# Optimization experiments

Measured on AMD Instinct MI355X. Metric: run time of the kernel, lower is better.

Reference implementation:

```python
import jax, jax.numpy as jnp
import numpy as np

N = 100000      # nodes
E = 1200000     # edges
F_IN = 256      # features_num
HID = 64        # hidden_dim = max(64, 2*32)
NC = 32         # num_class
H = 2           # GAT heads (edge_num < 1.4M)
GAT_SLOPE = 0.2 # GATConv internal LeakyReLU
ACT_SLOPE = 0.01  # F.leaky_relu default


def _glorot(k, shape):
    lim = float(np.sqrt(6.0 / (shape[0] + shape[-1])))
    return jax.random.uniform(k, shape, minval=-lim, maxval=lim, dtype=jnp.float32)


def setup_inputs() -> dict:
    key = jax.random.key(0)
    ks = jax.random.split(key, 32)
    inp = {
        "x": jax.random.normal(ks[0], (N, F_IN), dtype=jnp.float32),
        "edge_index": jax.random.randint(ks[1], (2, E), 0, N, dtype=jnp.int32),
        "edge_weight": jax.random.uniform(ks[2], (E,), dtype=jnp.float32),
    }
    in_dims = [F_IN, 3 * HID]  # layer2 input is cell.output_dim = HID*(1+H)
    ki = 3
    for l, d in enumerate(in_dims):
        inp[f"pre_W{l}"] = _glorot(ks[ki], (d, HID)); ki += 1
        inp[f"pre_b{l}"] = jnp.zeros((HID,), jnp.float32)
        inp[f"gat_W{l}"] = _glorot(ks[ki], (HID, H * HID)); ki += 1
        inp[f"att_src{l}"] = _glorot(ks[ki], (H, HID)); ki += 1
        inp[f"att_dst{l}"] = _glorot(ks[ki], (H, HID)); ki += 1
        inp[f"gat_b{l}"] = jnp.zeros((H * HID,), jnp.float32)
        inp[f"sg_W{l}"] = _glorot(ks[ki], (HID, HID)); ki += 1
        inp[f"sg_b{l}"] = jnp.zeros((HID,), jnp.float32)
    inp["cls_W"] = _glorot(ks[ki], (3 * HID, NC))
    inp["cls_b"] = jnp.zeros((NC,), jnp.float32)
    return inp


def _gat_conv(x, src, dst, W, att_src, att_dst, b):
    # src/dst already include self-loops. x: [N, HID]
    xp = (x @ W).reshape(N, H, HID)                       # [N, H, C]
    a_src = jnp.sum(xp * att_src, axis=-1)                # [N, H]
    a_dst = jnp.sum(xp * att_dst, axis=-1)                # [N, H]
    e = jax.nn.leaky_relu(a_src[src] + a_dst[dst], GAT_SLOPE)  # [E', H]
    m = jax.ops.segment_max(e, dst, num_segments=N)       # segment softmax over dst
    e = jnp.exp(e - m[dst])
    s = jax.ops.segment_sum(e, dst, num_segments=N)
    alpha = e / (s[dst] + 1e-16)
    out = jax.ops.segment_sum(xp[src] * alpha[:, :, None], dst, num_segments=N)
    return out.reshape(N, H * HID) + b


def _sg_conv(x, src_sl, dst_sl, w_sl, W, b):
    # gcn_norm with self-loops (weight 1) already appended; K=1 propagation then linear
    deg = jax.ops.segment_sum(w_sl, dst_sl, num_segments=N)
    dinv = jnp.where(deg > 0, jax.lax.rsqrt(deg), 0.0)
    norm = dinv[src_sl] * w_sl * dinv[dst_sl]             # [E']
    h = jax.ops.segment_sum(x[src_sl] * norm[:, None], dst_sl, num_segments=N)
    return h @ W + b


def _forward(x, edge_index, edge_weight, params):
    src, dst = edge_index[0], edge_index[1]
    loop = jnp.arange(N, dtype=src.dtype)
    src_sl = jnp.concatenate([src, loop])
    dst_sl = jnp.concatenate([dst, loop])
    w_sl = jnp.concatenate([edge_weight, jnp.ones((N,), edge_weight.dtype)])
    for l in range(2):
        pre_W, pre_b, gat_W, a_s, a_d, gat_b, sg_W, sg_b = params[l]
        xh = x @ pre_W + pre_b                            # preprocessor_x
        o1 = jax.nn.leaky_relu(_gat_conv(xh, src_sl, dst_sl, gat_W, a_s, a_d, gat_b), ACT_SLOPE)
        o2 = jax.nn.leaky_relu(_sg_conv(xh, src_sl, dst_sl, w_sl, sg_W, sg_b), ACT_SLOPE)
        x = jax.nn.relu(jnp.concatenate([o1, o2], axis=1))  # [N, 3*HID]
    cls_W, cls_b = params[2]
    logits = x @ cls_W + cls_b
    return jax.nn.log_softmax(logits, axis=-1)


def reference(x, edge_index, edge_weight,
              pre_W0, pre_b0, gat_W0, att_src0, att_dst0, gat_b0, sg_W0, sg_b0,
              pre_W1, pre_b1, gat_W1, att_src1, att_dst1, gat_b1, sg_W1, sg_b1,
              cls_W, cls_b):
    params = [
        (pre_W0, pre_b0, gat_W0, att_src0, att_dst0, gat_b0, sg_W0, sg_b0),
        (pre_W1, pre_b1, gat_W1, att_src1, att_dst1, gat_b1, sg_W1, sg_b1),
        (cls_W, cls_b),
    ]
    return _forward(x, edge_index, edge_weight, params)
```

## Files before the change

### kernel.cpp

```cpp
#include <hip/hip_runtime.h>
#include <hip/hip_fp16.h>
#include <math.h>

#define NN 100000
#define NE 1200000
#define FIN 256
#define NBLK 391
#define HB 4688
#define WB 170
#define GB64 1563

using half8   = __attribute__((ext_vector_type(8))) _Float16;
using floatx4 = __attribute__((ext_vector_type(4))) float;

__device__ __forceinline__ floatx4 mfma16(half8 a, half8 b, floatx4 c) {
    return __builtin_amdgcn_mfma_f32_16x16x32_f16(a, b, c, 0, 0, 0);
}

__device__ __forceinline__ void pre_epi(floatx4* acc, const float* b, const float* attf,
                                        float* asd, float* a_dst, __half* out,
                                        int rowb, int q, int n) {
    float vs0[4] = {0,0,0,0}, vs1[4] = {0,0,0,0};
    float vd0[4] = {0,0,0,0}, vd1[4] = {0,0,0,0};
    #pragma unroll
    for (int t = 0; t < 4; ++t) {
        float bb  = b[t * 16 + n];
        float ws0 = attf[t * 16 + n],       ws1 = attf[64 + t * 16 + n];
        float wd0 = attf[128 + t * 16 + n], wd1 = attf[192 + t * 16 + n];
        #pragma unroll
        for (int r = 0; r < 4; ++r) {
            float xv = acc[t][r] + bb;
            int row = rowb + q * 4 + r;
            if (row < NN) out[(size_t)row * 64 + t * 16 + n] = __float2half(xv);
            vs0[r] = fmaf(xv, ws0, vs0[r]);
            vs1[r] = fmaf(xv, ws1, vs1[r]);
            vd0[r] = fmaf(xv, wd0, vd0[r]);
            vd1[r] = fmaf(xv, wd1, vd1[r]);
        }
    }
    #pragma unroll
    for (int off = 1; off < 16; off <<= 1) {
        #pragma unroll
        for (int r = 0; r < 4; ++r) {
            vs0[r] += __shfl_xor(vs0[r], off);
            vs1[r] += __shfl_xor(vs1[r], off);
            vd0[r] += __shfl_xor(vd0[r], off);
            vd1[r] += __shfl_xor(vd1[r], off);
        }
    }
    if (n == 0) {
        #pragma unroll
        for (int r = 0; r < 4; ++r) {
            int row = rowb + q * 4 + r;
            if (row < NN) {
                *(float2*)&asd[row * 4] = make_float2(vs0[r], vs1[r]);
                *(float2*)&a_dst[row * 2] = make_float2(vd0[r], vd1[r]);
            }
        }
    }
}

__global__ __launch_bounds__(256) void k_prep(const int* __restrict__ dst,
                                              const float* __restrict__ ew,
                                              unsigned long long* __restrict__ packed,
                                              int* __restrict__ ord,
                                              const float* __restrict__ x,
                                              const float* __restrict__ W0,
                                              const float* __restrict__ W1,
                                              const float* __restrict__ Wg0,
                                              const float* __restrict__ Ws0,
                                              const float* __restrict__ Wg1,
                                              const float* __restrict__ Ws1,
                                              const float* __restrict__ Wc,
                                              const float* __restrict__ As0,
                                              const float* __restrict__ Ad0,
                                              const float* __restrict__ As1,
                                              const float* __restrict__ Ad1,
                                              const float* __restrict__ pre_b0,
                                              __half* __restrict__ Wf,
                                              float* __restrict__ attf,
                                              float* __restrict__ asd,
                                              float* __restrict__ a_dst,
                                              __half* __restrict__ xh) {
    __shared__ __half Wl[16384];
    __shared__ float attL[256];
    int bid = blockIdx.x;
    int tid = threadIdx.x;
    if (bid < HB) {
        int e = bid * 256 + tid;
        if (e >= NE) return;
        int d = dst[e]; float w = ew[e];
        unsigned long long add = (1ULL << 48)
            + (unsigned long long)((double)w * 4294967296.0);
        unsigned long long old = atomicAdd(&packed[d], add);
        ord[e] = (int)(old >> 48);
        return;
    }
    if (bid < HB + WB) {
        int o = (bid - HB) * 256 + tid + 16384;
        if (o >= 59904) return;
        if (o >= 59392) {
            int idx = o - 59392;
            int layer = idx >> 8, rem = idx & 255;
            int v = rem >> 6, c = rem & 63, h = v & 1;
            const float* Wg = layer ? Wg1 : Wg0;
            const float* av = (v < 2) ? (layer ? As1 : As0) : (layer ? Ad1 : Ad0);
            float s = 0.f;
            for (int jj = 0; jj < 64; ++jj)
                s = fmaf(Wg[c * 128 + h * 64 + jj], av[h * 64 + jj], s);
            attf[idx] = s;
            return;
        }
        int lo, NT, N; const float* Wg; const float* Wsg = nullptr;
        if (o < 28672)      { lo = o - 16384; NT = 4;  N = 64; Wg = W1; }
        else if (o < 40960) { lo = o - 28672; NT = 12; N = 0;  Wg = Wg0; Wsg = Ws0; }
        else if (o < 53248) { lo = o - 40960; NT = 12; N = 0;  Wg = Wg1; Wsg = Ws1; }
        else                { lo = o - 53248; NT = 2;  N = 32; Wg = Wc; }
        int j = lo & 7, n = (lo >> 3) & 15, q = (lo >> 7) & 3, rest = lo >> 9;
        int t = rest % NT, kc = rest / NT;
        int k = kc * 32 + q * 8 + j, col = t * 16 + n;
        float v;
        if (Wsg) v = (col < 128) ? Wg[(size_t)k * 128 + col] : Wsg[(size_t)k * 64 + (col - 128)];
        else     v = Wg[(size_t)k * N + col];
        Wf[o] = __float2half(v);
        return;
    }
    int pb = bid - (HB + WB);
    for (int i = tid; i < 16384; i += 256) {
        int j = i & 7, n = (i >> 3) & 15, q = (i >> 7) & 3, rest = i >> 9;
        int t = rest & 3, kc = rest >> 2;
        int k = kc * 32 + q * 8 + j, col = t * 16 + n;
        Wl[i] = __float2half(W0[(size_t)k * 64 + col]);
    }
    {
        int v = tid >> 6, c = tid & 63, h = v & 1;
        const float* av = (v < 2) ? As0 : Ad0;
        float s = 0.f;
        for (int jj = 0; jj < 64; ++jj)
            s = fmaf(Wg0[c * 128 + h * 64 + jj], av[h * 64 + jj], s);
        attL[tid] = s;
    }
    __syncthreads();
    int lane = tid & 63, wvv = tid >> 6;
    int q = lane >> 4, n = lane & 15;
    int rowb = pb * 64 + wvv * 16;
    int rowA = rowb + n; if (rowA > NN - 1) rowA = NN - 1;
    floatx4 acc[4] = {};
    const float* ap = x + (size_t)rowA * FIN + q * 8;
    const __half* wp = Wl + q * 128 + n * 8;
    #pragma unroll
    for (int kc = 0; kc < FIN / 32; ++kc) {
        float4 f0 = *(const float4*)(ap + kc * 32);
        float4 f1 = *(const float4*)(ap + kc * 32 + 4);
        half8 a;
        a[0] = (_Float16)f0.x; a[1] = (_Float16)f0.y;
        a[2] = (_Float16)f0.z; a[3] = (_Float16)f0.w;
        a[4] = (_Float16)f1.x; a[5] = (_Float16)f1.y;
        a[6] = (_Float16)f1.z; a[7] = (_Float16)f1.w;
        #pragma unroll
        for (int t = 0; t < 4; ++t) {
            half8 bf = *(const half8*)(wp + (size_t)(kc * 4 + t) * 512);
            acc[t] = mfma16(a, bf, acc[t]);
        }
    }
    pre_epi(acc, pre_b0, attL, asd, a_dst, xh, rowb, q, n);
}

__global__ __launch_bounds__(256) void k_scan(const unsigned long long* __restrict__ packed,
                                              int* __restrict__ row_ptr,
                                              float* __restrict__ asd,
                                              unsigned long long* __restrict__ desc) {
    __shared__ int tmp[256];
    __shared__ int exoff_sh;
    int tid = threadIdx.x, bid = blockIdx.x;
    int i = bid * 256 + tid;
    int v = 0;
    if (i < NN) {
        unsigned long long p = packed[i];
        v = (int)(p >> 48);
        double deg = (double)(p & 0xFFFFFFFFFFFFULL) * (1.0 / 4294967296.0) + 1.0;
        asd[i * 4 + 2] = rsqrtf((float)deg);
    }
    tmp[tid] = v;
    __syncthreads();
    for (int off = 1; off < 256; off <<= 1) {
        int t = (tid >= off) ? tmp[tid - off] : 0;
        __syncthreads();
        tmp[tid] += t;
        __syncthreads();
    }
    int bsum = tmp[255];
    if (bid == 0) {
        if (tid == 0) {
            exoff_sh = 0;
            atomicExch(&desc[0], (2ULL << 32) | (unsigned long long)(unsigned)bsum);
            row_ptr[NN] = NE;
        }
    } else if (tid < 64) {
        if (tid == 0)
            atomicExch(&desc[bid], (1ULL << 32) | (unsigned long long)(unsigned)bsum);
        int sum = 0;
        int base = bid - 1;
        for (;;) {
            int j = base - tid;
            unsigned long long d = 0;
            bool have = (j >= 0);
            if (have) {
                do { d = atomicAdd((unsigned long long*)&desc[j], 0ULL); }
                while ((d >> 32) == 0ULL);
            }
            unsigned long long m2 = __ballot(have && ((d >> 32) == 2ULL));
            if (m2) {
                int stop = __ffsll((long long)m2) - 1;
                if (tid <= stop) sum += (int)(d & 0xFFFFFFFFULL);
                break;
            }
            if (have) sum += (int)(d & 0xFFFFFFFFULL);
            base -= 64;
        }
        #pragma unroll
        for (int off = 32; off; off >>= 1) sum += __shfl_xor(sum, off);
        if (tid == 0) {
            exoff_sh = sum;
            atomicExch(&desc[bid],
                       (2ULL << 32) | (unsigned long long)(unsigned)(sum + bsum));
        }
    }
    __syncthreads();
    if (i < NN) row_ptr[i] = exoff_sh + tmp[tid] - v;
}

__global__ __launch_bounds__(256) void k_fill(const int* __restrict__ src,
                                              const int* __restrict__ dst,
                                              const float* __restrict__ ew,
                                              const int* __restrict__ row_ptr,
                                              const int* __restrict__ ord,
                                              int2* __restrict__ recs) {
    int e = blockIdx.x * 256 + threadIdx.x;
    if (e >= NE) return;
    int d = dst[e];
    int pos = row_ptr[d] + ord[e];
    int2 r; r.x = src[e]; r.y = __float_as_int(ew[e]);
    recs[pos] = r;
}

__global__ __launch_bounds__(256) void k_agg(const int* __restrict__ row_ptr,
                                             const int2* __restrict__ recs,
                                             const float* __restrict__ asd,
                                             const float* __restrict__ a_dst,
                                             const __half* __restrict__ xh,
                                             __half* __restrict__ agg) {
    __shared__ float4 einfo[4][64];
    int lane = threadIdx.x & 63;
    int wv = threadIdx.x >> 6;
    int d = blockIdx.x * 4 + wv;
    if (d >= NN) return;
    int p0 = row_ptr[d], p1 = row_ptr[d + 1];
    int nn = p1 - p0;
    float2 ad2 = ((const float2*)a_dst)[d];
    const float4* asd4 = (const float4*)asd;
    int sub = lane >> 5;
    unsigned flb = (unsigned)(lane & 31) * 4u;

    float g00 = 0.f, g01 = 0.f;
    float g10 = 0.f, g11 = 0.f;
    float s0a = 0.f, s1a = 0.f;

#define EDGE_ACC(E) do {                                                        \
        unsigned off_ = (unsigned)__float_as_int((E).w) + flb;                  \
        float2 v_ = __half22float2(*(const __half2*)((const char*)xh + off_));  \
        g00 = fmaf((E).x, v_.x, g00); g01 = fmaf((E).x, v_.y, g01);             \
        g10 = fmaf((E).y, v_.x, g10); g11 = fmaf((E).y, v_.y, g11);             \
        s0a = fmaf((E).z, v_.x, s0a); s1a = fmaf((E).z, v_.y, s1a);             \
    } while (0)

    if (nn <= 63) {
        int tot = nn + 1;
        float v0 = -INFINITY, v1 = -INFINITY, ewq = 0.f; int es = 0;
        if (lane < tot) {
            float wraw;
            if (lane < nn) {
                int2 rec = recs[p0 + lane];
                es = rec.x;
                wraw = __int_as_float(rec.y);
            } else { es = d; wraw = 1.f; }
            float4 a4 = asd4[es];
            v0 = a4.x + ad2.x; v0 = (v0 > 0.f) ? v0 : 0.2f * v0;
            v1 = a4.y + ad2.y; v1 = (v1 > 0.f) ? v1 : 0.2f * v1;
            ewq = wraw * a4.z;
        }
        float m0 = v0, m1 = v1;
        #pragma unroll
        for (int off = 32; off; off >>= 1) {
            m0 = fmaxf(m0, __shfl_xor(m0, off));
            m1 = fmaxf(m1, __shfl_xor(m1, off));
        }
        float e0 = (lane < tot) ? __expf(v0 - m0) : 0.f;
        float e1 = (lane < tot) ? __expf(v1 - m1) : 0.f;
        float s0 = e0, s1 = e1;
        #pragma unroll
        for (int off = 32; off; off >>= 1) {
            s0 += __shfl_xor(s0, off);
            s1 += __shfl_xor(s1, off);
        }
        if (lane < tot)
            einfo[wv][lane] = make_float4(e0 / (s0 + 1e-16f), e1 / (s1 + 1e-16f),
                                          ewq, __int_as_float(es << 7));
        const float4* ep = &einfo[wv][sub];
        int j = 0;
        for (; j + 4 <= tot; j += 4) {
            float4 eA = ep[j];
            float4 eB = ep[j + 2];
            EDGE_ACC(eA);
            EDGE_ACC(eB);
        }
        for (; j + 2 <= tot; j += 2) {
            float4 eA = ep[j];
            EDGE_ACC(eA);
        }
        if (tot & 1) {
            if (sub == 0) {
                float4 eT = einfo[wv][tot - 1];
                EDGE_ACC(eT);
            }
        }
    } else {
        float4 aself = asd4[d];
        float sv0 = aself.x + ad2.x; sv0 = (sv0 > 0.f) ? sv0 : 0.2f * sv0;
        float sv1 = aself.y + ad2.y; sv1 = (sv1 > 0.f) ? sv1 : 0.2f * sv1;
        float m0 = sv0, m1 = sv1;
        for (int e = p0 + lane; e < p1; e += 64) {
            int s = recs[e].x;
            float4 a4 = asd4[s];
            float v0 = a4.x + ad2.x; v0 = (v0 > 0.f) ? v0 : 0.2f * v0;
            float v1 = a4.y + ad2.y; v1 = (v1 > 0.f) ? v1 : 0.2f * v1;
            m0 = fmaxf(m0, v0); m1 = fmaxf(m1, v1);
        }
        #pragma unroll
        for (int off = 32; off; off >>= 1) {
            m0 = fmaxf(m0, __shfl_xor(m0, off));
            m1 = fmaxf(m1, __shfl_xor(m1, off));
        }
        float s0 = 0.f, s1 = 0.f;
        for (int e = p0 + lane; e < p1; e += 64) {
            int s = recs[e].x;
            float4 a4 = asd4[s];
            float v0 = a4.x + ad2.x; v0 = (v0 > 0.f) ? v0 : 0.2f * v0;
            float v1 = a4.y + ad2.y; v1 = (v1 > 0.f) ? v1 : 0.2f * v1;
            s0 += __expf(v0 - m0); s1 += __expf(v1 - m1);
        }
        #pragma unroll
        for (int off = 32; off; off >>= 1) {
            s0 += __shfl_xor(s0, off);
            s1 += __shfl_xor(s1, off);
        }
        s0 += __expf(sv0 - m0); s1 += __expf(sv1 - m1);
        float inv0 = 1.f / (s0 + 1e-16f), inv1 = 1.f / (s1 + 1e-16f);
        for (int base = p0; base < p1; base += 64) {
            int e = base + lane;
            int nc = min(64, p1 - base);
            if (e < p1) {
                int2 rec = recs[e];
                int es = rec.x;
                float4 a4 = asd4[es];
                float v0 = a4.x + ad2.x; v0 = (v0 > 0.f) ? v0 : 0.2f * v0;
                float v1 = a4.y + ad2.y; v1 = (v1 > 0.f) ? v1 : 0.2f * v1;
                einfo[wv][lane] = make_float4(__expf(v0 - m0) * inv0,
                                              __expf(v1 - m1) * inv1,
                                              __int_as_float(rec.y) * a4.z,
                                              __int_as_float(es << 7));
            }
            const float4* ep = &einfo[wv][sub];
            int j = 0;
            for (; j + 2 <= nc; j += 2) {
                float4 eA = ep[j];
                EDGE_ACC(eA);
            }
            if (nc & 1) {
                if (sub == 0) {
                    float4 eT = einfo[wv][nc - 1];
                    EDGE_ACC(eT);
                }
            }
        }
        if (sub == 0) {
            float4 eS = make_float4(__expf(sv0 - m0) * inv0,
                                    __expf(sv1 - m1) * inv1,
                                    aself.z, __int_as_float(d << 7));
            EDGE_ACC(eS);
        }
    }
#undef EDGE_ACC

    g00 += __shfl_xor(g00, 32); g01 += __shfl_xor(g01, 32);
    g10 += __shfl_xor(g10, 32); g11 += __shfl_xor(g11, 32);
    s0a += __shfl_xor(s0a, 32); s1a += __shfl_xor(s1a, 32);

    float did = asd[d * 4 + 2];
    __half* op = agg + (size_t)d * 192;
    int fp = (lane & 31) * 2;
    if (lane < 32) {
        *(__half2*)(op + fp)       = __floats2half2_rn(g00, g01);
        *(__half2*)(op + 128 + fp) = __floats2half2_rn(s0a * did, s1a * did);
    } else {
        *(__half2*)(op + 64 + fp)  = __floats2half2_rn(g10, g11);
    }
}

__global__ __launch_bounds__(256) void k_postpre(const __half* __restrict__ A,
                                                 const __half* __restrict__ Wfpq,
                                                 const float* __restrict__ gat_b,
                                                 const float* __restrict__ sg_b,
                                                 const __half* __restrict__ Wfpre,
                                                 const float* __restrict__ pre_b,
                                                 const float* __restrict__ attf,
                                                 float* __restrict__ asd,
                                                 float* __restrict__ a_dst,
                                                 __half* __restrict__ xh) {
    __shared__ __half tile[64][200];
    int lane = threadIdx.x & 63, wv = threadIdx.x >> 6;
    int q = lane >> 4, n = lane & 15;
    int rowb = blockIdx.x * 64 + wv * 16;
    int rowA = rowb + n; if (rowA > NN - 1) rowA = NN - 1;
    {
        floatx4 acc[12] = {};
        const __half* ap = A + (size_t)rowA * 192 + q * 8;
        const __half* wp = Wfpq + q * 128 + n * 8;
        #pragma unroll
        for (int g = 0; g < 3; ++g) {
            #pragma unroll
            for (int kc = 0; kc < 2; ++kc) {
                half8 a = *(const half8*)(ap + g * 64 + kc * 32);
                #pragma unroll
                for (int tt = 0; tt < 4; ++tt) {
                    int t = g * 4 + tt;
                    half8 bf = *(const half8*)(wp + (size_t)(kc * 12 + t) * 512);
                    acc[t] = mfma16(a, bf, acc[t]);
                }
            }
        }
        #pragma unroll
        for (int t = 0; t < 12; ++t) {
            float bb = (t < 8) ? gat_b[t * 16 + n] : sg_b[(t - 8) * 16 + n];
            #pragma unroll
            for (int r = 0; r < 4; ++r) {
                int row = rowb + q * 4 + r;
                float v = fmaxf(acc[t][r] + bb, 0.f);
                tile[wv * 16 + q * 4 + r][t * 16 + n] =
                    (row < NN) ? __float2half(v) : __half(0.f);
            }
        }
    }
    __syncthreads();
    {
        floatx4 acc[4] = {};
        const __half* ap2 = &tile[wv * 16 + n][q * 8];
        const __half* wp = Wfpre + q * 128 + n * 8;
        #pragma unroll
        for (int kc = 0; kc < 6; ++kc) {
            half8 a = *(const half8*)(ap2 + kc * 32);
            #pragma unroll
            for (int t = 0; t < 4; ++t) {
                half8 bf = *(const half8*)(wp + (size_t)(kc * 4 + t) * 512);
                acc[t] = mfma16(a, bf, acc[t]);
            }
        }
        pre_epi(acc, pre_b, attf, asd, a_dst, xh, rowb, q, n);
    }
}

__global__ __launch_bounds__(256) void k_postcls(const __half* __restrict__ A,
                                                 const __half* __restrict__ Wfpq,
                                                 const float* __restrict__ gat_b,
                                                 const float* __restrict__ sg_b,
                                                 const __half* __restrict__ Wfcls,
                                                 const float* __restrict__ b,
                                                 float* __restrict__ out) {
    __shared__ __half tile[64][200];
    int lane = threadIdx.x & 63, wv = threadIdx.x >> 6;
    int q = lane >> 4, n = lane & 15;
    int rowb = blockIdx.x * 64 + wv * 16;
    int rowA = rowb + n; if (rowA > NN - 1) rowA = NN - 1;
    {
        floatx4 acc[12] = {};
        const __half* ap = A + (size_t)rowA * 192 + q * 8;
        const __half* wp = Wfpq + q * 128 + n * 8;
        #pragma unroll
        for (int g = 0; g < 3; ++g) {
            #pragma unroll
            for (int kc = 0; kc < 2; ++kc) {
                half8 a = *(const half8*)(ap + g * 64 + kc * 32);
                #pragma unroll
                for (int tt = 0; tt < 4; ++tt) {
                    int t = g * 4 + tt;
                    half8 bf = *(const half8*)(wp + (size_t)(kc * 12 + t) * 512);
                    acc[t] = mfma16(a, bf, acc[t]);
                }
            }
        }
        #pragma unroll
        for (int t = 0; t < 12; ++t) {
            float bb = (t < 8) ? gat_b[t * 16 + n] : sg_b[(t - 8) * 16 + n];
            #pragma unroll
            for (int r = 0; r < 4; ++r) {
                int row = rowb + q * 4 + r;
                float v = fmaxf(acc[t][r] + bb, 0.f);
                tile[wv * 16 + q * 4 + r][t * 16 + n] =
                    (row < NN) ? __float2half(v) : __half(0.f);
            }
        }
    }
    __syncthreads();
    {
        floatx4 acc[2] = {};
        const __half* ap2 = &tile[wv * 16 + n][q * 8];
        const __half* wp = Wfcls + q * 128 + n * 8;
        #pragma unroll
        for (int kc = 0; kc < 6; ++kc) {
            half8 a = *(const half8*)(ap2 + kc * 32);
            #pragma unroll
            for (int t = 0; t < 2; ++t) {
                half8 bf = *(const half8*)(wp + (size_t)(kc * 2 + t) * 512);
                acc[t] = mfma16(a, bf, acc[t]);
            }
        }
        float b0 = b[n], b1 = b[16 + n];
        #pragma unroll
        for (int r = 0; r < 4; ++r) {
            float v0 = acc[0][r] + b0, v1 = acc[1][r] + b1;
            float mx = fmaxf(v0, v1);
            #pragma unroll
            for (int off = 1; off < 16; off <<= 1) mx = fmaxf(mx, __shfl_xor(mx, off));
            float sm = __expf(v0 - mx) + __expf(v1 - mx);
            #pragma unroll
            for (int off = 1; off < 16; off <<= 1) sm += __shfl_xor(sm, off);
            float lg = mx + __logf(sm);
            int row = rowb + q * 4 + r;
            if (row < NN) {
                out[(size_t)row * 32 + n]      = v0 - lg;
                out[(size_t)row * 32 + 16 + n] = v1 - lg;
            }
        }
    }
}

extern "C" void kernel_launch(void* const* d_in, const int* in_sizes, int n_in,
                              void* d_out, int out_size, void* d_ws, size_t ws_size,
                              hipStream_t stream) {
    const float* x   = (const float*)d_in[0];
    const int*   ei  = (const int*)d_in[1];
    const float* ew  = (const float*)d_in[2];
    const int* src = ei;
    const int* dst = ei + NE;

    const float* P[2][8];
    for (int l = 0; l < 2; ++l)
        for (int j = 0; j < 8; ++j)
            P[l][j] = (const float*)d_in[3 + l * 8 + j];
    const float* cls_W = (const float*)d_in[19];
    const float* cls_b = (const float*)d_in[20];

    float* ws = (float*)d_ws;
    const size_t n = NN;
    __half* xh_h = (__half*)(ws);
    __half* agg  = (__half*)(ws + 32 * n);
    float* asd   = ws + 128 * n;
    float* a_dst = ws + 132 * n;
    __half* Wf   = (__half*)(ws + 134 * n);
    float* attf  = ws + 134 * n + 29696;
    float* base2 = ws + 134 * n + 30208;
    unsigned long long* packed = (unsigned long long*)base2;
    unsigned long long* desc   = packed + NN;
    int*   row_ptr    = (int*)(desc + NBLK);
    int*   ord        = row_ptr + (NN + 2);
    int2*  recs       = (int2*)(ord + NE);

    __half* Wf_pre1 = Wf + 16384;
    __half* Wf_pq0  = Wf + 28672;
    __half* Wf_pq1  = Wf + 40960;
    __half* Wf_cls  = Wf + 53248;

    const int TB = 256;
    int gb_edge  = (NE + TB - 1) / TB;
    int gb_wave4 = (NN + 3) / 4;

    hipMemsetAsync(packed, 0, (NN + NBLK) * sizeof(unsigned long long), stream);
    k_prep<<<HB + WB + GB64, TB, 0, stream>>>(
        dst, ew, packed, ord, x,
        P[0][0], P[1][0], P[0][2], P[0][6], P[1][2], P[1][6], cls_W,
        P[0][3], P[0][4], P[1][3], P[1][4], P[0][1],
        Wf, attf, asd, a_dst, xh_h);

    k_scan<<<NBLK, TB, 0, stream>>>(packed, row_ptr, asd, desc);
    k_fill<<<gb_edge, TB, 0, stream>>>(src, dst, ew, row_ptr, ord, recs);

    k_agg    <<<gb_wave4, TB, 0, stream>>>(row_ptr, recs, asd, a_dst, xh_h, agg);
    k_postpre<<<GB64, TB, 0, stream>>>(agg, Wf_pq0, P[0][5], P[0][7],
                                       Wf_pre1, P[1][1], attf + 256,
                                       asd, a_dst, xh_h);
    k_agg    <<<gb_wave4, TB, 0, stream>>>(row_ptr, recs, asd, a_dst, xh_h, agg);
    k_postcls<<<GB64, TB, 0, stream>>>(agg, Wf_pq1, P[1][5], P[1][7],
                                       Wf_cls, cls_b, (float*)d_out);
}
```

Before: 482.7 us.

## Fuse edge aggregation into per-layer GEMM kernels and hoist W0 conversion

```diff
diff --git a/kernel.cpp b/kernel.cpp
--- a/kernel.cpp
+++ b/kernel.cpp
@@ -7,7 +7,7 @@
 #define FIN 256
 #define NBLK 391
 #define HB 4688
-#define WB 170
+#define WB2 170
 #define GB64 1563
 
 using half8   = __attribute__((ext_vector_type(8))) _Float16;
@@ -15,6 +15,15 @@
 
 __device__ __forceinline__ floatx4 mfma16(half8 a, half8 b, floatx4 c) {
     return __builtin_amdgcn_mfma_f32_16x16x32_f16(a, b, c, 0, 0, 0);
+}
+
+__global__ __launch_bounds__(256) void k_wpre0(const float* __restrict__ W0,
+                                               __half* __restrict__ Wf) {
+    int o = blockIdx.x * 256 + threadIdx.x;
+    int j = o & 7, n = (o >> 3) & 15, q = (o >> 7) & 3, rest = o >> 9;
+    int t = rest & 3, kc = rest >> 2;
+    int k = kc * 32 + q * 8 + j, col = t * 16 + n;
+    Wf[o] = __float2half(W0[(size_t)k * 64 + col]);
 }
 
 __device__ __forceinline__ void pre_epi(floatx4* acc, const float* b, const float* attf,
@@ -65,7 +74,7 @@
                                               unsigned long long* __restrict__ packed,
                                               int* __restrict__ ord,
                                               const float* __restrict__ x,
-                                              const float* __restrict__ W0,
+                                              const float* __restrict__ pre_b0,
                                               const float* __restrict__ W1,
                                               const float* __restrict__ Wg0,
                                               const float* __restrict__ Ws0,
@@ -76,28 +85,27 @@
                                               const float* __restrict__ Ad0,
                                               const float* __restrict__ As1,
                                               const float* __restrict__ Ad1,
-                                              const float* __restrict__ pre_b0,
                                               __half* __restrict__ Wf,
                                               float* __restrict__ attf,
-                                              float* __restrict__ asd,
-                                              float* __restrict__ a_dst,
-                                              __half* __restrict__ xh) {
-    __shared__ __half Wl[16384];
+                                              float* __restrict__ asd0,
+                                              float* __restrict__ adst0,
+                                              __half* __restrict__ xh0) {
     __shared__ float attL[256];
     int bid = blockIdx.x;
     int tid = threadIdx.x;
-    if (bid < HB) {
-        int e = bid * 256 + tid;
-        if (e >= NE) return;
-        int d = dst[e]; float w = ew[e];
-        unsigned long long add = (1ULL << 48)
-            + (unsigned long long)((double)w * 4294967296.0);
-        unsigned long long old = atomicAdd(&packed[d], add);
-        ord[e] = (int)(old >> 48);
-        return;
-    }
-    if (bid < HB + WB) {
-        int o = (bid - HB) * 256 + tid + 16384;
+    if (bid >= GB64) {
+        int b2 = bid - GB64;
+        if (b2 < HB) {
+            int e = b2 * 256 + tid;
+            if (e >= NE) return;
+            int d = dst[e]; float w = ew[e];
+            unsigned long long add = (1ULL << 48)
+                + (unsigned long long)((double)w * 4294967296.0);
+            unsigned long long old = atomicAdd(&packed[d], add);
+            ord[e] = (int)(old >> 48);
+            return;
+        }
+        int o = (b2 - HB) * 256 + tid + 16384;
         if (o >= 59904) return;
         if (o >= 59392) {
             int idx = o - 59392;
@@ -125,13 +133,6 @@
         Wf[o] = __float2half(v);
         return;
     }
-    int pb = bid - (HB + WB);
-    for (int i = tid; i < 16384; i += 256) {
-        int j = i & 7, n = (i >> 3) & 15, q = (i >> 7) & 3, rest = i >> 9;
-        int t = rest & 3, kc = rest >> 2;
-        int k = kc * 32 + q * 8 + j, col = t * 16 + n;
-        Wl[i] = __float2half(W0[(size_t)k * 64 + col]);
-    }
     {
         int v = tid >> 6, c = tid & 63, h = v & 1;
         const float* av = (v < 2) ? As0 : Ad0;
@@ -141,13 +142,13 @@
         attL[tid] = s;
     }
     __syncthreads();
-    int lane = tid & 63, wvv = tid >> 6;
+    int lane = tid & 63, wv = tid >> 6;
     int q = lane >> 4, n = lane & 15;
-    int rowb = pb * 64 + wvv * 16;
+    int rowb = bid * 64 + wv * 16;
     int rowA = rowb + n; if (rowA > NN - 1) rowA = NN - 1;
     floatx4 acc[4] = {};
     const float* ap = x + (size_t)rowA * FIN + q * 8;
-    const __half* wp = Wl + q * 128 + n * 8;
+    const __half* wp = Wf + q * 128 + n * 8;
     #pragma unroll
     for (int kc = 0; kc < FIN / 32; ++kc) {
         float4 f0 = *(const float4*)(ap + kc * 32);
@@ -163,12 +164,13 @@
             acc[t] = mfma16(a, bf, acc[t]);
         }
     }
-    pre_epi(acc, pre_b0, attL, asd, a_dst, xh, rowb, q, n);
+    pre_epi(acc, pre_b0, attL, asd0, adst0, xh0, rowb, q, n);
 }
 
 __global__ __launch_bounds__(256) void k_scan(const unsigned long long* __restrict__ packed,
                                               int* __restrict__ row_ptr,
-                                              float* __restrict__ asd,
+                                              float* __restrict__ asd0,
+                                              float* __restrict__ asd1,
                                               unsigned long long* __restrict__ desc) {
     __shared__ int tmp[256];
     __shared__ int exoff_sh;
@@ -179,7 +181,9 @@
         unsigned long long p = packed[i];
         v = (int)(p >> 48);
         double deg = (double)(p & 0xFFFFFFFFFFFFULL) * (1.0 / 4294967296.0) + 1.0;
-        asd[i * 4 + 2] = rsqrtf((float)deg);
+        float r = rsqrtf((float)deg);
+        asd0[i * 4 + 2] = r;
+        asd1[i * 4 + 2] = r;
     }
     tmp[tid] = v;
     __syncthreads();
@@ -244,23 +248,17 @@
     recs[pos] = r;
 }
 
-__global__ __launch_bounds__(256) void k_agg(const int* __restrict__ row_ptr,
-                                             const int2* __restrict__ recs,
-                                             const float* __restrict__ asd,
-                                             const float* __restrict__ a_dst,
-                                             const __half* __restrict__ xh,
-                                             __half* __restrict__ agg) {
-    __shared__ float4 einfo[4][64];
-    int lane = threadIdx.x & 63;
-    int wv = threadIdx.x >> 6;
-    int d = blockIdx.x * 4 + wv;
-    if (d >= NN) return;
+__device__ __forceinline__ void agg_node(int d, int lane, int sub, unsigned flb,
+                                         const int* __restrict__ row_ptr,
+                                         const int2* __restrict__ recs,
+                                         const float4* __restrict__ asd4,
+                                         const float* __restrict__ a_dst,
+                                         const __half* __restrict__ xh,
+                                         float4* __restrict__ einfoW,
+                                         __half* __restrict__ trow) {
     int p0 = row_ptr[d], p1 = row_ptr[d + 1];
     int nn = p1 - p0;
     float2 ad2 = ((const float2*)a_dst)[d];
-    const float4* asd4 = (const float4*)asd;
-    int sub = lane >> 5;
-    unsigned flb = (unsigned)(lane & 31) * 4u;
 
     float g00 = 0.f, g01 = 0.f;
     float g10 = 0.f, g11 = 0.f;
@@ -304,9 +302,9 @@
             s1 += __shfl_xor(s1, off);
         }
         if (lane < tot)
-            einfo[wv][lane] = make_float4(e0 / (s0 + 1e-16f), e1 / (s1 + 1e-16f),
-                                          ewq, __int_as_float(es << 7));
-        const float4* ep = &einfo[wv][sub];
+            einfoW[lane] = make_float4(e0 / (s0 + 1e-16f), e1 / (s1 + 1e-16f),
+                                       ewq, __int_as_float(es << 7));
+        const float4* ep = einfoW + sub;
         int j = 0;
         for (; j + 4 <= tot; j += 4) {
             float4 eA = ep[j];
@@ -320,7 +318,7 @@
         }
         if (tot & 1) {
             if (sub == 0) {
-                float4 eT = einfo[wv][tot - 1];
+                float4 eT = einfoW[tot - 1];
                 EDGE_ACC(eT);
             }
         }
@@ -365,12 +363,12 @@
                 float4 a4 = asd4[es];
                 float v0 = a4.x + ad2.x; v0 = (v0 > 0.f) ? v0 : 0.2f * v0;
                 float v1 = a4.y + ad2.y; v1 = (v1 > 0.f) ? v1 : 0.2f * v1;
-                einfo[wv][lane] = make_float4(__expf(v0 - m0) * inv0,
-                                              __expf(v1 - m1) * inv1,
-                                              __int_as_float(rec.y) * a4.z,
-                                              __int_as_float(es << 7));
-            }
-            const float4* ep = &einfo[wv][sub];
+                einfoW[lane] = make_float4(__expf(v0 - m0) * inv0,
+                                           __expf(v1 - m1) * inv1,
+                                           __int_as_float(rec.y) * a4.z,
+                                           __int_as_float(es << 7));
+            }
+            const float4* ep = einfoW + sub;
             int j = 0;
             for (; j + 2 <= nc; j += 2) {
                 float4 eA = ep[j];
@@ -378,7 +376,7 @@
             }
             if (nc & 1) {
                 if (sub == 0) {
-                    float4 eT = einfo[wv][nc - 1];
+                    float4 eT = einfoW[nc - 1];
                     EDGE_ACC(eT);
                 }
             }
@@ -396,35 +394,52 @@
     g10 += __shfl_xor(g10, 32); g11 += __shfl_xor(g11, 32);
     s0a += __shfl_xor(s0a, 32); s1a += __shfl_xor(s1a, 32);
 
-    float did = asd[d * 4 + 2];
-    __half* op = agg + (size_t)d * 192;
+    float did = asd4[d].z;
     int fp = (lane & 31) * 2;
     if (lane < 32) {
-        *(__half2*)(op + fp)       = __floats2half2_rn(g00, g01);
-        *(__half2*)(op + 128 + fp) = __floats2half2_rn(s0a * did, s1a * did);
+        *(__half2*)(trow + fp)       = __floats2half2_rn(g00, g01);
+        *(__half2*)(trow + 128 + fp) = __floats2half2_rn(s0a * did, s1a * did);
     } else {
-        *(__half2*)(op + 64 + fp)  = __floats2half2_rn(g10, g11);
-    }
-}
-
-__global__ __launch_bounds__(256) void k_postpre(const __half* __restrict__ A,
-                                                 const __half* __restrict__ Wfpq,
-                                                 const float* __restrict__ gat_b,
-                                                 const float* __restrict__ sg_b,
-                                                 const __half* __restrict__ Wfpre,
-                                                 const float* __restrict__ pre_b,
-                                                 const float* __restrict__ attf,
-                                                 float* __restrict__ asd,
-                                                 float* __restrict__ a_dst,
-                                                 __half* __restrict__ xh) {
+        *(__half2*)(trow + 64 + fp)  = __floats2half2_rn(g10, g11);
+    }
+}
+
+__global__ __launch_bounds__(256) void k_lay0(const int* __restrict__ row_ptr,
+                                              const int2* __restrict__ recs,
+                                              const float* __restrict__ asd_in,
+                                              const float* __restrict__ adst_in,
+                                              const __half* __restrict__ xh_in,
+                                              const __half* __restrict__ Wfpq,
+                                              const float* __restrict__ gat_b,
+                                              const float* __restrict__ sg_b,
+                                              const __half* __restrict__ Wfpre,
+                                              const float* __restrict__ pre_b,
+                                              const float* __restrict__ attf,
+                                              float* __restrict__ asd_out,
+                                              float* __restrict__ adst_out,
+                                              __half* __restrict__ xh_out) {
     __shared__ __half tile[64][200];
+    __shared__ float4 einfo[4][64];
     int lane = threadIdx.x & 63, wv = threadIdx.x >> 6;
+    int sub = lane >> 5;
+    unsigned flb = (unsigned)(lane & 31) * 4u;
+    const float4* asd4 = (const float4*)asd_in;
+    int base = blockIdx.x * 64 + wv * 16;
+    for (int i = 0; i < 16; ++i) {
+        int d = base + i;
+        __half* trow = &tile[wv * 16 + i][0];
+        if (d < NN) {
+            agg_node(d, lane, sub, flb, row_ptr, recs, asd4, adst_in, xh_in,
+                     einfo[wv], trow);
+        } else {
+            for (int c = lane; c < 192; c += 64) trow[c] = __float2half(0.f);
+        }
+    }
     int q = lane >> 4, n = lane & 15;
-    int rowb = blockIdx.x * 64 + wv * 16;
-    int rowA = rowb + n; if (rowA > NN - 1) rowA = NN - 1;
+    int rowb = base;
     {
         floatx4 acc[12] = {};
-        const __half* ap = A + (size_t)rowA * 192 + q * 8;
+        const __half* ap = &tile[wv * 16 + n][q * 8];
         const __half* wp = Wfpq + q * 128 + n * 8;
         #pragma unroll
         for (int g = 0; g < 3; ++g) {
@@ -444,14 +459,11 @@
             float bb = (t < 8) ? gat_b[t * 16 + n] : sg_b[(t - 8) * 16 + n];
             #pragma unroll
             for (int r = 0; r < 4; ++r) {
-                int row = rowb + q * 4 + r;
                 float v = fmaxf(acc[t][r] + bb, 0.f);
-                tile[wv * 16 + q * 4 + r][t * 16 + n] =
-                    (row < NN) ? __float2half(v) : __half(0.f);
-            }
-        }
-    }
-    __syncthreads();
+                tile[wv * 16 + q * 4 + r][t * 16 + n] = __float2half(v);
+            }
+        }
+    }
     {
         floatx4 acc[4] = {};
         const __half* ap2 = &tile[wv * 16 + n][q * 8];
@@ -465,25 +477,43 @@
                 acc[t] = mfma16(a, bf, acc[t]);
             }
         }
-        pre_epi(acc, pre_b, attf, asd, a_dst, xh, rowb, q, n);
-    }
-}
-
-__global__ __launch_bounds__(256) void k_postcls(const __half* __restrict__ A,
-                                                 const __half* __restrict__ Wfpq,
-                                                 const float* __restrict__ gat_b,
-                                                 const float* __restrict__ sg_b,
-                                                 const __half* __restrict__ Wfcls,
-                                                 const float* __restrict__ b,
-                                                 float* __restrict__ out) {
+        pre_epi(acc, pre_b, attf, asd_out, adst_out, xh_out, rowb, q, n);
+    }
+}
+
+__global__ __launch_bounds__(256) void k_lay1(const int* __restrict__ row_ptr,
+                                              const int2* __restrict__ recs,
+                                              const float* __restrict__ asd_in,
+                                              const float* __restrict__ adst_in,
+                                              const __half* __restrict__ xh_in,
+                                              const __half* __restrict__ Wfpq,
+                                              const float* __restrict__ gat_b,
+                                              const float* __restrict__ sg_b,
+                                              const __half* __restrict__ Wfcls,
+                                              const float* __restrict__ cb,
+                                              float* __restrict__ out) {
     __shared__ __half tile[64][200];
+    __shared__ float4 einfo[4][64];
     int lane = threadIdx.x & 63, wv = threadIdx.x >> 6;
+    int sub = lane >> 5;
+    unsigned flb = (unsigned)(lane & 31) * 4u;
+    const float4* asd4 = (const float4*)asd_in;
+    int base = blockIdx.x * 64 + wv * 16;
+    for (int i = 0; i < 16; ++i) {
+        int d = base + i;
+        __half* trow = &tile[wv * 16 + i][0];
+        if (d < NN) {
+            agg_node(d, lane, sub, flb, row_ptr, recs, asd4, adst_in, xh_in,
+                     einfo[wv], trow);
+        } else {
+            for (int c = lane; c < 192; c += 64) trow[c] = __float2half(0.f);
+        }
+    }
     int q = lane >> 4, n = lane & 15;
-    int rowb = blockIdx.x * 64 + wv * 16;
-    int rowA = rowb + n; if (rowA > NN - 1) rowA = NN - 1;
+    int rowb = base;
     {
         floatx4 acc[12] = {};
-        const __half* ap = A + (size_t)rowA * 192 + q * 8;
+        const __half* ap = &tile[wv * 16 + n][q * 8];
         const __half* wp = Wfpq + q * 128 + n * 8;
         #pragma unroll
         for (int g = 0; g < 3; ++g) {
@@ -503,14 +533,11 @@
             float bb = (t < 8) ? gat_b[t * 16 + n] : sg_b[(t - 8) * 16 + n];
             #pragma unroll
             for (int r = 0; r < 4; ++r) {
-                int row = rowb + q * 4 + r;
                 float v = fmaxf(acc[t][r] + bb, 0.f);
-                tile[wv * 16 + q * 4 + r][t * 16 + n] =
-                    (row < NN) ? __float2half(v) : __half(0.f);
-            }
-        }
-    }
-    __syncthreads();
+                tile[wv * 16 + q * 4 + r][t * 16 + n] = __float2half(v);
+            }
+        }
+    }
     {
         floatx4 acc[2] = {};
         const __half* ap2 = &tile[wv * 16 + n][q * 8];
@@ -524,7 +551,7 @@
                 acc[t] = mfma16(a, bf, acc[t]);
             }
         }
-        float b0 = b[n], b1 = b[16 + n];
+        float b0 = cb[n], b1 = cb[16 + n];
         #pragma unroll
         for (int r = 0; r < 4; ++r) {
             float v0 = acc[0][r] + b0, v1 = acc[1][r] + b1;
@@ -562,13 +589,15 @@
 
     float* ws = (float*)d_ws;
     const size_t n = NN;
-    __half* xh_h = (__half*)(ws);
-    __half* agg  = (__half*)(ws + 32 * n);
-    float* asd   = ws + 128 * n;
-    float* a_dst = ws + 132 * n;
-    __half* Wf   = (__half*)(ws + 134 * n);
-    float* attf  = ws + 134 * n + 29696;
-    float* base2 = ws + 134 * n + 30208;
+    __half* xh0  = (__half*)(ws);
+    __half* xh1  = (__half*)(ws + 32 * n);
+    float* asd0  = ws + 64 * n;
+    float* asd1  = ws + 68 * n;
+    float* adst0 = ws + 72 * n;
+    float* adst1 = ws + 74 * n;
+    __half* Wf   = (__half*)(ws + 76 * n);
+    float* attf  = ws + 76 * n + 29696;
+    float* base2 = ws + 76 * n + 30208;
     unsigned long long* packed = (unsigned long long*)base2;
     unsigned long long* desc   = packed + NN;
     int*   row_ptr    = (int*)(desc + NBLK);
@@ -581,24 +610,24 @@
     __half* Wf_cls  = Wf + 53248;
 
     const int TB = 256;
-    int gb_edge  = (NE + TB - 1) / TB;
-    int gb_wave4 = (NN + 3) / 4;
 
     hipMemsetAsync(packed, 0, (NN + NBLK) * sizeof(unsigned long long), stream);
-    k_prep<<<HB + WB + GB64, TB, 0, stream>>>(
-        dst, ew, packed, ord, x,
-        P[0][0], P[1][0], P[0][2], P[0][6], P[1][2], P[1][6], cls_W,
-        P[0][3], P[0][4], P[1][3], P[1][4], P[0][1],
-        Wf, attf, asd, a_dst, xh_h);
-
-    k_scan<<<NBLK, TB, 0, stream>>>(packed, row_ptr, asd, desc);
-    k_fill<<<gb_edge, TB, 0, stream>>>(src, dst, ew, row_ptr, ord, recs);
-
-    k_agg    <<<gb_wave4, TB, 0, stream>>>(row_ptr, recs, asd, a_dst, xh_h, agg);
-    k_postpre<<<GB64, TB, 0, stream>>>(agg, Wf_pq0, P[0][5], P[0][7],
-                                       Wf_pre1, P[1][1], attf + 256,
-                                       asd, a_dst, xh_h);
-    k_agg    <<<gb_wave4, TB, 0, stream>>>(row_ptr, recs, asd, a_dst, xh_h, agg);
-    k_postcls<<<GB64, TB, 0, stream>>>(agg, Wf_pq1, P[1][5], P[1][7],
-                                       Wf_cls, cls_b, (float*)d_out);
-}
+    k_wpre0<<<64, TB, 0, stream>>>(P[0][0], Wf);
+
+    k_prep<<<GB64 + HB + WB2, TB, 0, stream>>>(
+        dst, ew, packed, ord, x, P[0][1],
+        P[1][0], P[0][2], P[0][6], P[1][2], P[1][6], cls_W,
+        P[0][3], P[0][4], P[1][3], P[1][4],
+        Wf, attf, asd0, adst0, xh0);
+
+    k_scan<<<NBLK, TB, 0, stream>>>(packed, row_ptr, asd0, asd1, desc);
+    k_fill<<<HB, TB, 0, stream>>>(src, dst, ew, row_ptr, ord, recs);
+
+    k_lay0<<<GB64, TB, 0, stream>>>(row_ptr, recs, asd0, adst0, xh0,
+                                    Wf_pq0, P[0][5], P[0][7],
+                                    Wf_pre1, P[1][1], attf + 256,
+                                    asd1, adst1, xh1);
+    k_lay1<<<GB64, TB, 0, stream>>>(row_ptr, recs, asd1, adst1, xh1,
+                                    Wf_pq1, P[1][5], P[1][7],
+                                    Wf_cls, cls_b, (float*)d_out);
+}
```

Result: slower. 638.4 us (+32.3%).

## Split W0 conversion into separate kernel and widen per-lane features in aggregation

Applied to the files above, without the earlier changes.

```diff
diff --git a/kernel.cpp b/kernel.cpp
--- a/kernel.cpp
+++ b/kernel.cpp
@@ -7,7 +7,7 @@
 #define FIN 256
 #define NBLK 391
 #define HB 4688
-#define WB 170
+#define WB2 170
 #define GB64 1563
 
 using half8   = __attribute__((ext_vector_type(8))) _Float16;
@@ -15,6 +15,15 @@
 
 __device__ __forceinline__ floatx4 mfma16(half8 a, half8 b, floatx4 c) {
     return __builtin_amdgcn_mfma_f32_16x16x32_f16(a, b, c, 0, 0, 0);
+}
+
+__global__ __launch_bounds__(256) void k_wpre0(const float* __restrict__ W0,
+                                               __half* __restrict__ Wf) {
+    int o = blockIdx.x * 256 + threadIdx.x;
+    int j = o & 7, n = (o >> 3) & 15, q = (o >> 7) & 3, rest = o >> 9;
+    int t = rest & 3, kc = rest >> 2;
+    int k = kc * 32 + q * 8 + j, col = t * 16 + n;
+    Wf[o] = __float2half(W0[(size_t)k * 64 + col]);
 }
 
 __device__ __forceinline__ void pre_epi(floatx4* acc, const float* b, const float* attf,
@@ -65,7 +74,7 @@
                                               unsigned long long* __restrict__ packed,
                                               int* __restrict__ ord,
                                               const float* __restrict__ x,
-                                              const float* __restrict__ W0,
+                                              const float* __restrict__ pre_b0,
                                               const float* __restrict__ W1,
                                               const float* __restrict__ Wg0,
                                               const float* __restrict__ Ws0,
@@ -76,28 +85,27 @@
                                               const float* __restrict__ Ad0,
                                               const float* __restrict__ As1,
                                               const float* __restrict__ Ad1,
-                                              const float* __restrict__ pre_b0,
                                               __half* __restrict__ Wf,
                                               float* __restrict__ attf,
                                               float* __restrict__ asd,
                                               float* __restrict__ a_dst,
                                               __half* __restrict__ xh) {
-    __shared__ __half Wl[16384];
     __shared__ float attL[256];
     int bid = blockIdx.x;
     int tid = threadIdx.x;
-    if (bid < HB) {
-        int e = bid * 256 + tid;
-        if (e >= NE) return;
-        int d = dst[e]; float w = ew[e];
-        unsigned long long add = (1ULL << 48)
-            + (unsigned long long)((double)w * 4294967296.0);
-        unsigned long long old = atomicAdd(&packed[d], add);
-        ord[e] = (int)(old >> 48);
-        return;
-    }
-    if (bid < HB + WB) {
-        int o = (bid - HB) * 256 + tid + 16384;
+    if (bid >= GB64) {
+        int b2 = bid - GB64;
+        if (b2 < HB) {
+            int e = b2 * 256 + tid;
+            if (e >= NE) return;
+            int d = dst[e]; float w = ew[e];
+            unsigned long long add = (1ULL << 48)
+                + (unsigned long long)((double)w * 4294967296.0);
+            unsigned long long old = atomicAdd(&packed[d], add);
+            ord[e] = (int)(old >> 48);
+            return;
+        }
+        int o = (b2 - HB) * 256 + tid + 16384;
         if (o >= 59904) return;
         if (o >= 59392) {
             int idx = o - 59392;
@@ -125,13 +133,6 @@
         Wf[o] = __float2half(v);
         return;
     }
-    int pb = bid - (HB + WB);
-    for (int i = tid; i < 16384; i += 256) {
-        int j = i & 7, n = (i >> 3) & 15, q = (i >> 7) & 3, rest = i >> 9;
-        int t = rest & 3, kc = rest >> 2;
-        int k = kc * 32 + q * 8 + j, col = t * 16 + n;
-        Wl[i] = __float2half(W0[(size_t)k * 64 + col]);
-    }
     {
         int v = tid >> 6, c = tid & 63, h = v & 1;
         const float* av = (v < 2) ? As0 : Ad0;
@@ -141,13 +142,13 @@
         attL[tid] = s;
     }
     __syncthreads();
-    int lane = tid & 63, wvv = tid >> 6;
+    int lane = tid & 63, wv = tid >> 6;
     int q = lane >> 4, n = lane & 15;
-    int rowb = pb * 64 + wvv * 16;
+    int rowb = bid * 64 + wv * 16;
     int rowA = rowb + n; if (rowA > NN - 1) rowA = NN - 1;
     floatx4 acc[4] = {};
     const float* ap = x + (size_t)rowA * FIN + q * 8;
-    const __half* wp = Wl + q * 128 + n * 8;
+    const __half* wp = Wf + q * 128 + n * 8;
     #pragma unroll
     for (int kc = 0; kc < FIN / 32; ++kc) {
         float4 f0 = *(const float4*)(ap + kc * 32);
@@ -259,19 +260,25 @@
     int nn = p1 - p0;
     float2 ad2 = ((const float2*)a_dst)[d];
     const float4* asd4 = (const float4*)asd;
-    int sub = lane >> 5;
-    unsigned flb = (unsigned)(lane & 31) * 4u;
-
-    float g00 = 0.f, g01 = 0.f;
-    float g10 = 0.f, g11 = 0.f;
-    float s0a = 0.f, s1a = 0.f;
+    float4* einfoW = einfo[wv];
+    int sub4 = lane >> 4;
+    unsigned flb = (unsigned)(lane & 15) * 8u;
+
+    float g00 = 0.f, g01 = 0.f, g02 = 0.f, g03 = 0.f;
+    float g10 = 0.f, g11 = 0.f, g12 = 0.f, g13 = 0.f;
+    float sa0 = 0.f, sa1 = 0.f, sa2 = 0.f, sa3 = 0.f;
 
 #define EDGE_ACC(E) do {                                                        \
         unsigned off_ = (unsigned)__float_as_int((E).w) + flb;                  \
-        float2 v_ = __half22float2(*(const __half2*)((const char*)xh + off_));  \
-        g00 = fmaf((E).x, v_.x, g00); g01 = fmaf((E).x, v_.y, g01);             \
-        g10 = fmaf((E).y, v_.x, g10); g11 = fmaf((E).y, v_.y, g11);             \
-        s0a = fmaf((E).z, v_.x, s0a); s1a = fmaf((E).z, v_.y, s1a);             \
+        float2 raw_ = *(const float2*)((const char*)xh + off_);                 \
+        float2 f0_ = __half22float2(*(__half2*)&raw_.x);                        \
+        float2 f1_ = __half22float2(*(__half2*)&raw_.y);                        \
+        g00 = fmaf((E).x, f0_.x, g00); g01 = fmaf((E).x, f0_.y, g01);           \
+        g02 = fmaf((E).x, f1_.x, g02); g03 = fmaf((E).x, f1_.y, g03);           \
+        g10 = fmaf((E).y, f0_.x, g10); g11 = fmaf((E).y, f0_.y, g11);           \
+        g12 = fmaf((E).y, f1_.x, g12); g13 = fmaf((E).y, f1_.y, g13);           \
+        sa0 = fmaf((E).z, f0_.x, sa0); sa1 = fmaf((E).z, f0_.y, sa1);           \
+        sa2 = fmaf((E).z, f1_.x, sa2); sa3 = fmaf((E).z, f1_.y, sa3);           \
     } while (0)
 
     if (nn <= 63) {
@@ -304,25 +311,23 @@
             s1 += __shfl_xor(s1, off);
         }
         if (lane < tot)
-            einfo[wv][lane] = make_float4(e0 / (s0 + 1e-16f), e1 / (s1 + 1e-16f),
-                                          ewq, __int_as_float(es << 7));
-        const float4* ep = &einfo[wv][sub];
+            einfoW[lane] = make_float4(e0 / (s0 + 1e-16f), e1 / (s1 + 1e-16f),
+                                       ewq, __int_as_float(es << 7));
+        const float4* ep = einfoW + sub4;
         int j = 0;
+        for (; j + 8 <= tot; j += 8) {
+            float4 eA = ep[j];
+            float4 eB = ep[j + 4];
+            EDGE_ACC(eA);
+            EDGE_ACC(eB);
+        }
         for (; j + 4 <= tot; j += 4) {
             float4 eA = ep[j];
-            float4 eB = ep[j + 2];
             EDGE_ACC(eA);
-            EDGE_ACC(eB);
-        }
-        for (; j + 2 <= tot; j += 2) {
-            float4 eA = ep[j];
-            EDGE_ACC(eA);
-        }
-        if (tot & 1) {
-            if (sub == 0) {
-                float4 eT = einfo[wv][tot - 1];
-                EDGE_ACC(eT);
-            }
+        }
+        if (sub4 < tot - j) {
+            float4 eT = ep[j];
+            EDGE_ACC(eT);
         }
     } else {
         float4 aself = asd4[d];
@@ -365,25 +370,23 @@
                 float4 a4 = asd4[es];
                 float v0 = a4.x + ad2.x; v0 = (v0 > 0.f) ? v0 : 0.2f * v0;
                 float v1 = a4.y + ad2.y; v1 = (v1 > 0.f) ? v1 : 0.2f * v1;
-                einfo[wv][lane] = make_float4(__expf(v0 - m0) * inv0,
-                                              __expf(v1 - m1) * inv1,
-                                              __int_as_float(rec.y) * a4.z,
-                                              __int_as_float(es << 7));
-            }
-            const float4* ep = &einfo[wv][sub];
+                einfoW[lane] = make_float4(__expf(v0 - m0) * inv0,
+                                           __expf(v1 - m1) * inv1,
+                                           __int_as_float(rec.y) * a4.z,
+                                           __int_as_float(es << 7));
+            }
+            const float4* ep = einfoW + sub4;
             int j = 0;
-            for (; j + 2 <= nc; j += 2) {
+            for (; j + 4 <= nc; j += 4) {
                 float4 eA = ep[j];
                 EDGE_ACC(eA);
             }
-            if (nc & 1) {
-                if (sub == 0) {
-                    float4 eT = einfo[wv][nc - 1];
-                    EDGE_ACC(eT);
-                }
-            }
-        }
-        if (sub == 0) {
+            if (sub4 < nc - j) {
+                float4 eT = ep[j];
+                EDGE_ACC(eT);
+            }
+        }
+        if (sub4 == 0) {
             float4 eS = make_float4(__expf(sv0 - m0) * inv0,
                                     __expf(sv1 - m1) * inv1,
                                     aself.z, __int_as_float(d << 7));
@@ -392,18 +395,28 @@
     }
 #undef EDGE_ACC
 
-    g00 += __shfl_xor(g00, 32); g01 += __shfl_xor(g01, 32);
-    g10 += __shfl_xor(g10, 32); g11 += __shfl_xor(g11, 32);
-    s0a += __shfl_xor(s0a, 32); s1a += __shfl_xor(s1a, 32);
-
-    float did = asd[d * 4 + 2];
+    #pragma unroll
+    for (int off = 16; off <= 32; off <<= 1) {
+        g00 += __shfl_xor(g00, off); g01 += __shfl_xor(g01, off);
+        g02 += __shfl_xor(g02, off); g03 += __shfl_xor(g03, off);
+        g10 += __shfl_xor(g10, off); g11 += __shfl_xor(g11, off);
+        g12 += __shfl_xor(g12, off); g13 += __shfl_xor(g13, off);
+        sa0 += __shfl_xor(sa0, off); sa1 += __shfl_xor(sa1, off);
+        sa2 += __shfl_xor(sa2, off); sa3 += __shfl_xor(sa3, off);
+    }
+
+    float did = asd4[d].z;
     __half* op = agg + (size_t)d * 192;
-    int fp = (lane & 31) * 2;
-    if (lane < 32) {
-        *(__half2*)(op + fp)       = __floats2half2_rn(g00, g01);
-        *(__half2*)(op + 128 + fp) = __floats2half2_rn(s0a * did, s1a * did);
-    } else {
-        *(__half2*)(op + 64 + fp)  = __floats2half2_rn(g10, g11);
+    int grp = lane >> 4, fo = (lane & 15) * 4;
+    __half2 lo, hi;
+    if (grp == 0)      { lo = __floats2half2_rn(g00, g01); hi = __floats2half2_rn(g02, g03); }
+    else if (grp == 1) { lo = __floats2half2_rn(g10, g11); hi = __floats2half2_rn(g12, g13); }
+    else               { lo = __floats2half2_rn(sa0 * did, sa1 * did);
+                         hi = __floats2half2_rn(sa2 * did, sa3 * did); }
+    if (grp < 3) {
+        uint2 u;
+        u.x = *(unsigned*)&lo; u.y = *(unsigned*)&hi;
+        *(uint2*)(op + grp * 64 + fo) = u;
     }
 }
 
@@ -581,18 +594,19 @@
     __half* Wf_cls  = Wf + 53248;
 
     const int TB = 256;
-    int gb_edge  = (NE + TB - 1) / TB;
     int gb_wave4 = (NN + 3) / 4;
 
     hipMemsetAsync(packed, 0, (NN + NBLK) * sizeof(unsigned long long), stream);
-    k_prep<<<HB + WB + GB64, TB, 0, stream>>>(
-        dst, ew, packed, ord, x,
-        P[0][0], P[1][0], P[0][2], P[0][6], P[1][2], P[1][6], cls_W,
-        P[0][3], P[0][4], P[1][3], P[1][4], P[0][1],
+    k_wpre0<<<64, TB, 0, stream>>>(P[0][0], Wf);
+
+    k_prep<<<GB64 + HB + WB2, TB, 0, stream>>>(
+        dst, ew, packed, ord, x, P[0][1],
+        P[1][0], P[0][2], P[0][6], P[1][2], P[1][6], cls_W,
+        P[0][3], P[0][4], P[1][3], P[1][4],
         Wf, attf, asd, a_dst, xh_h);
 
     k_scan<<<NBLK, TB, 0, stream>>>(packed, row_ptr, asd, desc);
-    k_fill<<<gb_edge, TB, 0, stream>>>(src, dst, ew, row_ptr, ord, recs);
+    k_fill<<<HB, TB, 0, stream>>>(src, dst, ew, row_ptr, ord, recs);
 
     k_agg    <<<gb_wave4, TB, 0, stream>>>(row_ptr, recs, asd, a_dst, xh_h, agg);
     k_postpre<<<GB64, TB, 0, stream>>>(agg, Wf_pq0, P[0][5], P[0][7],
```

New measurement: 466.7 us. 1.03x faster.
